# Kernel tuning notes

Measured on AMD Instinct MI355X. Metric: run time of the kernel, lower is better.

## Reference

```python
import jax, jax.numpy as jnp
import numpy as np

HEADS, DIM_HEAD, BITS = 12, 64, 4


def quantize(q, bits):
    # per-tensor affine fake-quant, exactly as the torch quantize()
    s = (q.max() - q.min()) / (2.0 ** bits - 1.0)
    z = jnp.round(2.0 ** bits - 1.0 - q.max() / s)
    return jnp.round(q / s + z), s, z


def setup_inputs() -> dict:
    key = jax.random.key(0)
    k1, k2, k3, k4 = jax.random.split(key, 4)
    return {
        "x": jax.random.normal(k1, (4, 1024, 768), jnp.float32),
        "w_qkv": jax.random.normal(k2, (2304, 768), jnp.float32) * 0.02,  # torch Linear weight [out,in]
        "w_out": jax.random.normal(k3, (768, 768), jnp.float32) * 0.02,
        "b_out": jax.random.normal(k4, (768,), jnp.float32) * 0.02,
    }


def reference(x, w_qkv, w_out, b_out):
    scale = DIM_HEAD ** -0.5
    B, N, D = x.shape
    # --- quantized QKV projection: x @ W^T with zero-point correction ---
    xq, sx1, zx1 = quantize(x, BITS)
    w1, sw1, zw1 = quantize(w_qkv.T, BITS)  # [D, 3*inner]
    xqkv = (xq @ w1
            - w1.sum(0, keepdims=True) * zx1
            - xq.sum(2, keepdims=True) * zw1
            + zx1 * zw1 * D) * (sx1 * sw1)  # [B, N, 3*inner]
    q, k, v = jnp.split(xqkv, 3, axis=-1)
    to_heads = lambda t: t.reshape(B, N, HEADS, DIM_HEAD).transpose(0, 2, 1, 3)  # b h n d
    q, k, v = to_heads(q), to_heads(k), to_heads(v)
    # --- quantized QK^T (note: original omits the +zq*zk*d term) ---
    qq, sq, zq = quantize(q, BITS)
    kq, sk, zk = quantize(k.transpose(0, 1, 3, 2), BITS)  # b h d n
    dots = (qq @ kq
            - kq.sum(2, keepdims=True) * zq
            - qq.sum(3, keepdims=True) * zk) * (scale * sq * sk)  # b h n n
    a = jax.nn.softmax(dots, axis=-1)
    # --- quantized A @ V ---
    aq, sa, za = quantize(a, BITS)
    vq, sv, zv = quantize(v, BITS)
    out = (aq @ vq
           - vq.sum(2, keepdims=True) * za
           - aq.sum(3, keepdims=True) * zv
           + za * zv * N) * (sa * sv)  # b h n d
    out = out.transpose(0, 2, 1, 3).reshape(B, N, HEADS * DIM_HEAD)
    # --- quantized output projection (faithful to original: correction uses
    # xqkv.sum / xqkv width, reproducing the source's use of `x` here) ---
    oq, sx2, zx2 = quantize(out, BITS)
    w2, sw2, zw2 = quantize(w_out.T, BITS)  # [inner, D]
    o = (oq @ w2
         - w2.sum(0, keepdims=True) * zx2
         - xqkv.sum(2, keepdims=True) * zw2
         + zx2 * zw2 * xqkv.shape[2]) * (sx2 * sw2) + b_out
    return o
```

## Files before the change

### kernel.cpp

```cpp
#include <hip/hip_runtime.h>
#include <math.h>

#define HEADS 12
#define DH    64
#define Dm    768
#define I3    2304
#define Nn    1024
#define Mm    4096
#define BHt   48
#define LOG2E 1.4426950408889634f

#define P_X  0
#define P_W1 1
#define P_Q  2
#define P_K  3
#define P_V  4
#define P_A  5
#define P_O  6
#define P_W2 7

typedef int v4i __attribute__((ext_vector_type(4)));

#if __has_builtin(__builtin_amdgcn_exp2f)
#define EXP2(x) __builtin_amdgcn_exp2f(x)
#else
#define EXP2(x) exp2f(x)
#endif

__device__ inline unsigned encf(float f) {
    unsigned u = __float_as_uint(f);
    return (u & 0x80000000u) ? ~u : (u | 0x80000000u);
}
__device__ inline float decf(unsigned u) {
    return (u & 0x80000000u) ? __uint_as_float(u & 0x7fffffffu) : __uint_as_float(~u);
}
__device__ inline void get_sz(const unsigned* scal, int pair, float* s, float* z) {
    float mn = decf(scal[2 * pair]);
    float mx = decf(scal[2 * pair + 1]);
    float ss = (mx - mn) / 15.0f;
    *s = ss;
    *z = rintf(15.0f - mx / ss);
}

__global__ __launch_bounds__(256) void k_init(unsigned* scal, float* z1, int n1, float* z2, int n2) {
    int g = blockIdx.x * 256 + threadIdx.x;
    if (g < n1) z1[g] = 0.f;
    if (g < n2) z2[g] = 0.f;
    if (g < 8) { scal[2 * g] = 0xFFFFFFFFu; scal[2 * g + 1] = 0u; }
}

__global__ __launch_bounds__(256) void k_minmax3(const float* x, const float* w1, const float* w2,
                                                 unsigned* scal) {
    __shared__ float rmn[256], rmx[256];
    int bid = blockIdx.x, tid = threadIdx.x;
    const float* src; int rows, pair, b0, nb;
    if (bid < 256)      { src = x;  rows = 4096; pair = P_X;  b0 = 0;   nb = 256; }
    else if (bid < 384) { src = w1; rows = 2304; pair = P_W1; b0 = 256; nb = 128; }
    else                { src = w2; rows = 768;  pair = P_W2; b0 = 384; nb = 64;  }
    float mn = INFINITY, mx = -INFINITY;
    for (int r = bid - b0; r < rows; r += nb) {
        const float* row = src + (long)r * 768;
#pragma unroll
        for (int k = 0; k < 3; ++k) {
            float v = row[tid + k * 256];
            mn = fminf(mn, v); mx = fmaxf(mx, v);
        }
    }
    rmn[tid] = mn; rmx[tid] = mx; __syncthreads();
    for (int s = 128; s > 0; s >>= 1) {
        if (tid < s) { rmn[tid] = fminf(rmn[tid], rmn[tid + s]); rmx[tid] = fmaxf(rmx[tid], rmx[tid + s]); }
        __syncthreads();
    }
    if (tid == 0) {
        atomicMin(&scal[2 * pair], encf(rmn[0]));
        atomicMax(&scal[2 * pair + 1], encf(rmx[0]));
    }
}

__global__ __launch_bounds__(256) void k_quant3(const float* x, const float* w1, const float* w2,
                                                const unsigned* scal,
                                                signed char* xq, signed char* wq, signed char* w2q,
                                                float* rs_x, float* rs_w1, float* rs_w2) {
    __shared__ float red[256];
    int bid = blockIdx.x, tid = threadIdx.x;
    const float* src; signed char* dq; float* rs; int pair, r;
    if (bid < 4096)      { src = x;  dq = xq;  rs = rs_x;  pair = P_X;  r = bid; }
    else if (bid < 6400) { src = w1; dq = wq;  rs = rs_w1; pair = P_W1; r = bid - 4096; }
    else                 { src = w2; dq = w2q; rs = rs_w2; pair = P_W2; r = bid - 6400; }
    float s, z; get_sz(scal, pair, &s, &z);
    const float* row = src + (long)r * 768;
    signed char* drow = dq + (long)r * 768;
    float acc = 0.f;
#pragma unroll
    for (int k = 0; k < 3; ++k) {
        int c = tid + k * 256;
        float q = rintf(row[c] / s + z);
        drow[c] = (signed char)(int)q;
        acc += q;
    }
    red[tid] = acc; __syncthreads();
    for (int s2 = 128; s2 > 0; s2 >>= 1) { if (tid < s2) red[tid] += red[tid + s2]; __syncthreads(); }
    if (tid == 0) rs[r] = red[0];
}

__global__ __launch_bounds__(256) void k_quant_rows(const float* src, const unsigned* scal, int pair,
                                                    signed char* dq) {
    int r = blockIdx.x, tid = threadIdx.x;
    float s, z; get_sz(scal, pair, &s, &z);
    const float* row = src + (long)r * 768;
    signed char* drow = dq + (long)r * 768;
#pragma unroll
    for (int k = 0; k < 3; ++k) {
        int c = tid + k * 256;
        float q = rintf(row[c] / s + z);
        drow[c] = (signed char)(int)q;
    }
}

__global__ __launch_bounds__(256) void k_gemm_mfma(const signed char* A, const signed char* B,
                                                   const float* colsumB, const float* rowsumA,
                                                   const float* bias, float* C, int K, int ldC,
                                                   const unsigned* scal, int pairA, int pairB,
                                                   float corrK, int do_stats, float* rowsum_out,
                                                   unsigned* scal_mm) {
    __shared__ __align__(16) signed char As[128 * 64];
    __shared__ __align__(16) signed char Bs[128 * 64];
    __shared__ float red[256];
    int tid = threadIdx.x;
    int wave = tid >> 6, lane = tid & 63;
    int col16 = lane & 15, quad = lane >> 4;
    long rowbase = (long)blockIdx.y * 128;
    long colbase = (long)blockIdx.x * 128;

    int c4 = tid & 3, r4 = tid >> 2;
    const signed char* ag0 = A + (rowbase + r4) * K + c4 * 16;
    const signed char* ag1 = A + (rowbase + r4 + 64) * K + c4 * 16;
    const signed char* bg0 = B + (colbase + r4) * K + c4 * 16;
    const signed char* bg1 = B + (colbase + r4 + 64) * K + c4 * 16;
    int soff0 = ((r4 >> 4) << 10) + (c4 << 8) + ((r4 & 15) << 4);
    int soff1 = soff0 + 4096;

    v4i ra0 = *(const v4i*)ag0;
    v4i ra1 = *(const v4i*)ag1;
    v4i rb0 = *(const v4i*)bg0;
    v4i rb1 = *(const v4i*)bg1;

    const int afrag_off = wave * 2048 + quad * 256 + col16 * 16;
    const int bfrag_off = quad * 256 + col16 * 16;
    v4i acc[2][8] = {};
    int nk = K >> 6;
    for (int kt = 0; kt < nk; ++kt) {
        *(v4i*)(As + soff0) = ra0;
        *(v4i*)(As + soff1) = ra1;
        *(v4i*)(Bs + soff0) = rb0;
        *(v4i*)(Bs + soff1) = rb1;
        __syncthreads();
        if (kt + 1 < nk) {
            int ko = (kt + 1) << 6;
            ra0 = *(const v4i*)(ag0 + ko);
            ra1 = *(const v4i*)(ag1 + ko);
            rb0 = *(const v4i*)(bg0 + ko);
            rb1 = *(const v4i*)(bg1 + ko);
        }
        v4i af0 = *(const v4i*)(As + afrag_off);
        v4i af1 = *(const v4i*)(As + afrag_off + 1024);
        v4i bf[8];
#pragma unroll
        for (int g = 0; g < 8; ++g) bf[g] = *(const v4i*)(Bs + bfrag_off + g * 1024);
#pragma unroll
        for (int g = 0; g < 8; ++g) {
            acc[0][g] = __builtin_amdgcn_mfma_i32_16x16x64_i8(af0, bf[g], acc[0][g], 0, 0, 0);
            acc[1][g] = __builtin_amdgcn_mfma_i32_16x16x64_i8(af1, bf[g], acc[1][g], 0, 0, 0);
        }
        __syncthreads();
    }

    float sA, zA, sB, zB;
    get_sz(scal, pairA, &sA, &zA);
    get_sz(scal, pairB, &sB, &zB);
    float sAB = sA * sB;
    float zz = (zA * zB) * corrK;
    float vmn = INFINITY, vmx = -INFINITY;
    float rowpart[2][4] = {};
#pragma unroll
    for (int i2 = 0; i2 < 2; ++i2)
#pragma unroll
        for (int g = 0; g < 8; ++g) {
            long col = colbase + g * 16 + col16;
            float cs = colsumB[col] * zA;
            float bv = bias ? bias[col] : 0.f;
#pragma unroll
            for (int r = 0; r < 4; ++r) {
                long row = rowbase + wave * 32 + i2 * 16 + quad * 4 + r;
                float v = ((float)acc[i2][g][r] - cs - rowsumA[row] * zB + zz) * sAB + bv;
                C[row * ldC + col] = v;
                rowpart[i2][r] += v;
                vmn = fminf(vmn, v); vmx = fmaxf(vmx, v);
            }
        }
    if (do_stats) {
#pragma unroll
        for (int i2 = 0; i2 < 2; ++i2)
#pragma unroll
            for (int r = 0; r < 4; ++r) {
                float s = rowpart[i2][r];
                s += __shfl_xor(s, 1); s += __shfl_xor(s, 2);
                s += __shfl_xor(s, 4); s += __shfl_xor(s, 8);
                if (col16 == 0)
                    atomicAdd(&rowsum_out[rowbase + wave * 32 + i2 * 16 + quad * 4 + r], s);
            }
        int pair = P_Q + (int)(colbase / 768);
        red[tid] = vmx; __syncthreads();
        for (int s = 128; s > 0; s >>= 1) { if (tid < s) red[tid] = fmaxf(red[tid], red[tid + s]); __syncthreads(); }
        if (tid == 0) atomicMax(&scal_mm[2 * pair + 1], encf(red[0]));
        __syncthreads();
        red[tid] = vmn; __syncthreads();
        for (int s = 128; s > 0; s >>= 1) { if (tid < s) red[tid] = fminf(red[tid], red[tid + s]); __syncthreads(); }
        if (tid == 0) atomicMin(&scal_mm[2 * pair], encf(red[0]));
    }
}

__global__ __launch_bounds__(256) void k_quant_qkv2(const float* xqkv, const unsigned* scal,
                                                    signed char* qq, signed char* kq, signed char* vqT,
                                                    float* rowsum_qq, float* cskc, float* colsum_vq) {
    __shared__ __align__(16) signed char vt[64 * 80];
    __shared__ float vred[4][64];
    int blk = blockIdx.x;
    int bh = blk >> 4, itile = blk & 15;
    int tid = threadIdx.x;
    int wave = tid >> 6, d = tid & 63;
    int b = bh / HEADS, h = bh - HEADS * b;
    float sq, zq, sk, zk, sv, zv;
    get_sz(scal, P_Q, &sq, &zq);
    get_sz(scal, P_K, &sk, &zk);
    get_sz(scal, P_V, &sv, &zv);
    float zqcsc2 = zq * ((0.125f * sq) * sk) * LOG2E;
    int vb = 0;
    float vsum = 0.f;
    for (int ir = 0; ir < 16; ++ir) {
        int il = wave * 16 + ir;
        int i = itile * 64 + il;
        const float* row = xqkv + ((long)b * Nn + i) * I3 + h * DH;
        float q = rintf(row[d] / sq + zq);
        float k = rintf(row[768 + d] / sk + zk);
        float v = rintf(row[1536 + d] / sv + zv);
        long o = ((long)bh * Nn + i) * 64 + d;
        qq[o] = (signed char)(int)q;
        kq[o] = (signed char)(int)k;
        vsum += v;
        vb |= ((int)v & 0xff) << ((ir & 3) * 8);
        if ((ir & 3) == 3) {
            *(int*)(vt + d * 80 + (il & ~3)) = vb;
            vb = 0;
        }
        float s1 = q, s2 = k;
        for (int off = 32; off > 0; off >>= 1) {
            s1 += __shfl_down(s1, off);
            s2 += __shfl_down(s2, off);
        }
        if (d == 0) { rowsum_qq[bh * Nn + i] = s1; cskc[bh * Nn + i] = s2 * zqcsc2; }
    }
    vred[wave][d] = vsum;
    __syncthreads();
    int dd = tid >> 2, c = tid & 3;
    *(v4i*)(vqT + ((long)bh * 64 + dd) * 1024 + itile * 64 + c * 16) = *(const v4i*)(vt + dd * 80 + c * 16);
    if (tid < 64)
        atomicAdd(&colsum_vq[bh * 64 + tid],
                  ((vred[0][tid] + vred[1][tid]) + vred[2][tid]) + vred[3][tid]);
}

__global__ __launch_bounds__(256) void k_attn_a8(const signed char* qq, const signed char* kq,
                                                 const float* rowsum_qq, const float* cskc,
                                                 unsigned* scal, float* rowmax, float* sumexp) {
    __shared__ float red[256];
    int blk = blockIdx.x;
    int bh = blk >> 4, itile = blk & 15;
    int tid = threadIdx.x;
    int wave = tid >> 6, lane = tid & 63;
    int col16 = lane & 15, quad = lane >> 4;
    int rowbase = itile * 64 + wave * 16;
    const signed char* kbase = kq + (long)bh * Nn * 64;
    const float* ck = cskc + bh * Nn;
    v4i afrag = *(const v4i*)(qq + ((long)bh * Nn + rowbase + col16) * 64 + quad * 16);
    float sq, zq, sk, zk;
    get_sz(scal, P_Q, &sq, &zq);
    get_sz(scal, P_K, &sk, &zk);
    float csc2 = ((0.125f * sq) * sk) * LOG2E;
    float rzc[4];
#pragma unroll
    for (int r = 0; r < 4; ++r)
        rzc[r] = rowsum_qq[bh * Nn + rowbase + quad * 4 + r] * zk * csc2;
    v4i zero = {0, 0, 0, 0};
    float m[4]    = {-INFINITY, -INFINITY, -INFINITY, -INFINITY};
    float se[4]   = {0.f, 0.f, 0.f, 0.f};
    float lmin[4] = {INFINITY, INFINITY, INFINITY, INFINITY};
    const signed char* kf = kbase + (long)col16 * 64 + quad * 16;
    const float* ckp = ck + col16;
    v4i kb[2][4];
    float ckc[4], ckn[4];
#pragma unroll
    for (int t = 0; t < 4; ++t) {
        kb[0][t] = *(const v4i*)(kf + (long)(t * 16) * 64);
        ckc[t] = ckp[t * 16];
    }
#pragma unroll 2
    for (int ch = 0; ch < 16; ++ch) {
        int cur = ch & 1, nxt = cur ^ 1;
        int pch = (ch < 15) ? ch + 1 : 15;
#pragma unroll
        for (int t = 0; t < 4; ++t) {
            kb[nxt][t] = *(const v4i*)(kf + (long)(pch * 64 + t * 16) * 64);
            ckn[t] = ckp[pch * 64 + t * 16];
        }
#pragma unroll
        for (int t = 0; t < 4; ++t) {
            v4i d = __builtin_amdgcn_mfma_i32_16x16x64_i8(afrag, kb[cur][t], zero, 0, 0, 0);
            float ckv = ckc[t];
#pragma unroll
            for (int r = 0; r < 4; ++r) {
                float dv = fmaf((float)d[r], csc2, -(ckv + rzc[r]));
                lmin[r] = fminf(lmin[r], dv);
                float mn = fmaxf(m[r], dv);
                float e = EXP2(fminf(m[r], dv) - mn);
                se[r] = (dv > m[r]) ? fmaf(se[r], e, 1.0f) : (se[r] + e);
                m[r] = mn;
            }
        }
#pragma unroll
        for (int t = 0; t < 4; ++t) ckc[t] = ckn[t];
    }
#pragma unroll
    for (int r = 0; r < 4; ++r) {
#pragma unroll
        for (int off = 1; off < 16; off <<= 1) {
            float mo = __shfl_xor(m[r], off);
            float so = __shfl_xor(se[r], off);
            float mino = __shfl_xor(lmin[r], off);
            float mn = fmaxf(m[r], mo);
            se[r] = fmaf(se[r], EXP2(m[r] - mn), so * EXP2(mo - mn));
            m[r] = mn;
            lmin[r] = fminf(lmin[r], mino);
        }
    }
    float amax_c = -INFINITY, amin_c = INFINITY;
    if (col16 == 0) {
#pragma unroll
        for (int r = 0; r < 4; ++r) {
            int grow = bh * Nn + rowbase + quad * 4 + r;
            rowmax[grow] = m[r];
            sumexp[grow] = se[r];
            amax_c = fmaxf(amax_c, 1.0f / se[r]);
            amin_c = fminf(amin_c, EXP2(lmin[r] - m[r]) / se[r]);
        }
    }
    red[tid] = amax_c; __syncthreads();
    for (int s = 128; s > 0; s >>= 1) { if (tid < s) red[tid] = fmaxf(red[tid], red[tid + s]); __syncthreads(); }
    if (tid == 0) atomicMax(&scal[2 * P_A + 1], encf(red[0]));
    __syncthreads();
    red[tid] = amin_c; __syncthreads();
    for (int s = 128; s > 0; s >>= 1) { if (tid < s) red[tid] = fminf(red[tid], red[tid + s]); __syncthreads(); }
    if (tid == 0) atomicMin(&scal[2 * P_A], encf(red[0]));
}

__global__ __launch_bounds__(256) void k_attn_b8(const signed char* qq, const signed char* kq,
                                                 const signed char* vqT, const float* rowsum_qq,
                                                 const float* cskc, const float* colsum_vq,
                                                 const float* rowmax, const float* sumexp,
                                                 unsigned* scal, float* out_mat) {
    __shared__ __align__(16) signed char AqB[8192];
    __shared__ float red[256];
    int blk = blockIdx.x;
    int bh = blk >> 4, itile = blk & 15;
    int tid = threadIdx.x;
    int wave = tid >> 6, lane = tid & 63;
    int col16 = lane & 15, quad = lane >> 4;
    int rowbase = itile * 64 + wave * 16;
    int b = bh / HEADS, h = bh - HEADS * b;
    const signed char* kbase = kq + (long)bh * Nn * 64;
    const signed char* vbase = vqT + (long)bh * 64 * 1024;
    const float* ck = cskc + bh * Nn;
    v4i afrag = *(const v4i*)(qq + ((long)bh * Nn + rowbase + col16) * 64 + quad * 16);
    float sq, zq, sk, zk, sv, zv, sa, za;
    get_sz(scal, P_Q, &sq, &zq);
    get_sz(scal, P_K, &sk, &zk);
    get_sz(scal, P_V, &sv, &zv);
    get_sz(scal, P_A, &sa, &za);
    float csc2 = ((0.125f * sq) * sk) * LOG2E;
    float roff[4], crcp[4];
#pragma unroll
    for (int r = 0; r < 4; ++r) {
        int row = bh * Nn + rowbase + quad * 4 + r;
        roff[r] = rowsum_qq[row] * zk * csc2 + rowmax[row];
        crcp[r] = 1.0f / (sumexp[row] * sa);
    }
    v4i accPV[4] = {};
    float rs_a[4] = {0.f, 0.f, 0.f, 0.f};
    v4i zero = {0, 0, 0, 0};
    const signed char* kf = kbase + (long)col16 * 64 + quad * 16;
    const float* ckp = ck + col16;
    const int pa_off = wave * 1024 + col16 * 64 + ((quad ^ (col16 >> 2)) << 4);

    v4i kb0[4], kb1[4];
    float ckr0[4], ckr1[4];
#pragma unroll
    for (int t = 0; t < 4; ++t) {
        kb0[t] = *(const v4i*)(kf + (long)(t * 16) * 64);
        ckr0[t] = ckp[t * 16];
        kb1[t] = *(const v4i*)(kf + (long)(64 + t * 16) * 64);
        ckr1[t] = ckp[64 + t * 16];
    }

#define QUANT_CHUNK(BUF, KB, CKR)                                                       \
    {                                                                                   \
        signed char* myAq = AqB + (BUF) * 4096 + wave * 1024;                           \
        _Pragma("unroll")                                                               \
        for (int t = 0; t < 4; ++t) {                                                   \
            v4i d = __builtin_amdgcn_mfma_i32_16x16x64_i8(afrag, KB[t], zero, 0, 0, 0); \
            float ckv = CKR[t];                                                         \
            int cswz = ((t ^ quad) << 4) + col16;                                       \
            _Pragma("unroll")                                                           \
            for (int r = 0; r < 4; ++r) {                                               \
                float es = fmaf((float)d[r], csc2, -(ckv + roff[r]));                   \
                float fastv = fmaf(EXP2(es), crcp[r], za);                              \
                float aqv = rintf(fastv);                                               \
                rs_a[r] += aqv;                                                         \
                myAq[(quad * 4 + r) * 64 + cswz] = (signed char)(int)aqv;               \
            }                                                                           \
        }                                                                               \
    }

#define BODY(CH, CUR, KBc, CKc, KBn, CKn)                                               \
    {                                                                                   \
        v4i pa = *(const v4i*)(AqB + (CUR) * 4096 + pa_off);                            \
        v4i bv[4];                                                                      \
        _Pragma("unroll")                                                               \
        for (int g = 0; g < 4; ++g)                                                     \
            bv[g] = *(const v4i*)(vbase + (long)(g * 16 + col16) * 1024 + (CH) * 64 + quad * 16); \
        if ((CH) < 14) {                                                                \
            _Pragma("unroll")                                                           \
            for (int t = 0; t < 4; ++t) {                                               \
                KBc[t] = *(const v4i*)(kf + (long)(((CH) + 2) * 64 + t * 16) * 64);     \
                CKc[t] = ckp[((CH) + 2) * 64 + t * 16];                                 \
            }                                                                           \
        }                                                                               \
        if ((CH) < 15) QUANT_CHUNK(1 - (CUR), KBn, CKn)                                 \
        _Pragma("unroll")                                                               \
        for (int g = 0; g < 4; ++g)                                                     \
            accPV[g] = __builtin_amdgcn_mfma_i32_16x16x64_i8(pa, bv[g], accPV[g], 0, 0, 0); \
    }

    QUANT_CHUNK(0, kb0, ckr0)
    for (int ch2 = 0; ch2 < 8; ++ch2) {
        int ch = ch2 * 2;
        BODY(ch, 0, kb0, ckr0, kb1, ckr1)
        BODY(ch + 1, 1, kb1, ckr1, kb0, ckr0)
    }
#undef BODY
#undef QUANT_CHUNK

#pragma unroll
    for (int r = 0; r < 4; ++r)
        for (int off = 1; off < 16; off <<= 1) rs_a[r] += __shfl_xor(rs_a[r], off);
    float sav = sa * sv;
    float zz = (za * zv) * 1024.0f;
    float vmn = INFINITY, vmx = -INFINITY;
#pragma unroll
    for (int g = 0; g < 4; ++g) {
        int d = g * 16 + col16;
        float cs = colsum_vq[bh * 64 + d] * za;
#pragma unroll
        for (int r = 0; r < 4; ++r) {
            int i = rowbase + quad * 4 + r;
            float v = ((float)accPV[g][r] - cs - rs_a[r] * zv + zz) * sav;
            out_mat[((long)b * Nn + i) * Dm + h * DH + d] = v;
            vmn = fminf(vmn, v); vmx = fmaxf(vmx, v);
        }
    }
    red[tid] = vmx; __syncthreads();
    for (int s = 128; s > 0; s >>= 1) { if (tid < s) red[tid] = fmaxf(red[tid], red[tid + s]); __syncthreads(); }
    if (tid == 0) atomicMax(&scal[2 * P_O + 1], encf(red[0]));
    __syncthreads();
    red[tid] = vmn; __syncthreads();
    for (int s = 128; s > 0; s >>= 1) { if (tid < s) red[tid] = fminf(red[tid], red[tid + s]); __syncthreads(); }
    if (tid == 0) atomicMin(&scal[2 * P_O], encf(red[0]));
}

extern "C" void kernel_launch(void* const* d_in, const int* in_sizes, int n_in,
                              void* d_out, int out_size, void* d_ws, size_t ws_size,
                              hipStream_t stream) {
    const float* x     = (const float*)d_in[0];
    const float* w_qkv = (const float*)d_in[1];
    const float* w_out = (const float*)d_in[2];
    const float* b_out = (const float*)d_in[3];

    char* ws = (char*)d_ws;
    size_t off = 0;
    auto alloc = [&](size_t n) -> char* {
        char* p = ws + off;
        off = (off + n + 255) & ~(size_t)255;
        return p;
    };
    unsigned*    scal        = (unsigned*)alloc(64);
    float*       xqkv        = (float*)alloc((size_t)Mm * I3 * 4);
    float*       out_mat     = (float*)alloc((size_t)Mm * Dm * 4);
    signed char* xq          = (signed char*)alloc((size_t)Mm * Dm);
    signed char* wq          = (signed char*)alloc((size_t)I3 * Dm);
    signed char* w2q         = (signed char*)alloc((size_t)Dm * Dm);
    signed char* oq          = (signed char*)alloc((size_t)Mm * Dm);
    signed char* qq          = (signed char*)alloc((size_t)BHt * Nn * DH);
    signed char* kq          = (signed char*)alloc((size_t)BHt * Nn * DH);
    signed char* vqT         = (signed char*)alloc((size_t)BHt * Nn * DH);
    float*       rowsum_xq   = (float*)alloc((size_t)Mm * 4);
    float*       colsum_w1   = (float*)alloc((size_t)I3 * 4);
    float*       colsum_w2   = (float*)alloc((size_t)Dm * 4);
    float*       rowsum_xqkv = (float*)alloc((size_t)Mm * 4);
    float*       rowsum_qq   = (float*)alloc((size_t)BHt * Nn * 4);
    float*       cskc        = (float*)alloc((size_t)BHt * Nn * 4);
    float*       colsum_vq   = (float*)alloc((size_t)BHt * DH * 4);
    float*       rowmax      = (float*)alloc((size_t)BHt * Nn * 4);
    float*       sumexp      = (float*)alloc((size_t)BHt * Nn * 4);

    k_init<<<28, 256, 0, stream>>>(scal, rowsum_xqkv, Mm, colsum_vq, BHt * DH);

    k_minmax3<<<448, 256, 0, stream>>>(x, w_qkv, w_out, scal);
    k_quant3<<<7168, 256, 0, stream>>>(x, w_qkv, w_out, scal, xq, wq, w2q,
                                       rowsum_xq, colsum_w1, colsum_w2);

    {
        dim3 g(I3 / 128, Mm / 128);
        k_gemm_mfma<<<g, 256, 0, stream>>>(xq, wq, colsum_w1, rowsum_xq, nullptr, xqkv,
                                           Dm, I3, scal, P_X, P_W1, 768.0f,
                                           1, rowsum_xqkv, scal);
    }

    k_quant_qkv2<<<BHt * 16, 256, 0, stream>>>(xqkv, scal, qq, kq, vqT,
                                               rowsum_qq, cskc, colsum_vq);

    k_attn_a8<<<BHt * 16, 256, 0, stream>>>(qq, kq, rowsum_qq, cskc, scal, rowmax, sumexp);
    k_attn_b8<<<BHt * 16, 256, 0, stream>>>(qq, kq, vqT, rowsum_qq, cskc, colsum_vq,
                                            rowmax, sumexp, scal, out_mat);

    k_quant_rows<<<Mm, 256, 0, stream>>>(out_mat, scal, P_O, oq);

    {
        dim3 g(Dm / 128, Mm / 128);
        k_gemm_mfma<<<g, 256, 0, stream>>>(oq, w2q, colsum_w2, rowsum_xqkv, b_out, (float*)d_out,
                                           Dm, Dm, scal, P_O, P_W2, 2304.0f,
                                           0, nullptr, nullptr);
    }
}
```

Baseline: 255.6 us.

## Split attention key range across wave pairs and double attention grid size

Both attention kernels now give each block 32 query rows instead of 64, with two waves per 16-row strip each covering half of the key columns. Partial softmax statistics and partial PV accumulators are merged through shared memory, which doubles the grid to 1536 blocks and halves the serial key loop per wave. Launch bounds now request higher occupancy. The cost is duplicated Q fragment loads, extra LDS traffic and barriers for the merge, and half the waves sitting idle during the output store.

```diff
diff --git a/kernel.cpp b/kernel.cpp
--- a/kernel.cpp
+++ b/kernel.cpp
@@ -269,16 +269,18 @@
                   ((vred[0][tid] + vred[1][tid]) + vred[2][tid]) + vred[3][tid]);
 }
 
-__global__ __launch_bounds__(256) void k_attn_a8(const signed char* qq, const signed char* kq,
+__global__ __launch_bounds__(256, 6) void k_attn_a8(const signed char* qq, const signed char* kq,
                                                  const float* rowsum_qq, const float* cskc,
                                                  unsigned* scal, float* rowmax, float* sumexp) {
     __shared__ float red[256];
+    __shared__ float Am[4][16], Ase[4][16], Almn[4][16];
     int blk = blockIdx.x;
-    int bh = blk >> 4, itile = blk & 15;
+    int bh = blk >> 5, itile = blk & 31;
     int tid = threadIdx.x;
     int wave = tid >> 6, lane = tid & 63;
     int col16 = lane & 15, quad = lane >> 4;
-    int rowbase = itile * 64 + wave * 16;
+    int rowbase = itile * 32 + (wave >> 1) * 16;
+    int c0 = (wave & 1) * 8;
     const signed char* kbase = kq + (long)bh * Nn * 64;
     const float* ck = cskc + bh * Nn;
     v4i afrag = *(const v4i*)(qq + ((long)bh * Nn + rowbase + col16) * 64 + quad * 16);
@@ -294,8 +296,8 @@
     float m[4]    = {-INFINITY, -INFINITY, -INFINITY, -INFINITY};
     float se[4]   = {0.f, 0.f, 0.f, 0.f};
     float lmin[4] = {INFINITY, INFINITY, INFINITY, INFINITY};
-    const signed char* kf = kbase + (long)col16 * 64 + quad * 16;
-    const float* ckp = ck + col16;
+    const signed char* kf = kbase + (long)(c0 * 64 + col16) * 64 + quad * 16;
+    const float* ckp = ck + c0 * 64 + col16;
     v4i kb[2][4];
     float ckc[4], ckn[4];
 #pragma unroll
@@ -304,9 +306,9 @@
         ckc[t] = ckp[t * 16];
     }
 #pragma unroll 2
-    for (int ch = 0; ch < 16; ++ch) {
+    for (int ch = 0; ch < 8; ++ch) {
         int cur = ch & 1, nxt = cur ^ 1;
-        int pch = (ch < 15) ? ch + 1 : 15;
+        int pch = (ch < 7) ? ch + 1 : 7;
 #pragma unroll
         for (int t = 0; t < 4; ++t) {
             kb[nxt][t] = *(const v4i*)(kf + (long)(pch * 64 + t * 16) * 64);
@@ -342,16 +344,27 @@
             lmin[r] = fminf(lmin[r], mino);
         }
     }
+    if (col16 == 0) {
+#pragma unroll
+        for (int r = 0; r < 4; ++r) {
+            Am[wave][quad * 4 + r]   = m[r];
+            Ase[wave][quad * 4 + r]  = se[r];
+            Almn[wave][quad * 4 + r] = lmin[r];
+        }
+    }
+    __syncthreads();
     float amax_c = -INFINITY, amin_c = INFINITY;
-    if (col16 == 0) {
-#pragma unroll
-        for (int r = 0; r < 4; ++r) {
-            int grow = bh * Nn + rowbase + quad * 4 + r;
-            rowmax[grow] = m[r];
-            sumexp[grow] = se[r];
-            amax_c = fmaxf(amax_c, 1.0f / se[r]);
-            amin_c = fminf(amin_c, EXP2(lmin[r] - m[r]) / se[r]);
-        }
+    if (tid < 32) {
+        int p = tid >> 4, row = tid & 15;
+        float m1 = Am[2 * p][row], m2 = Am[2 * p + 1][row];
+        float mm = fmaxf(m1, m2);
+        float ses = Ase[2 * p][row] * EXP2(m1 - mm) + Ase[2 * p + 1][row] * EXP2(m2 - mm);
+        float lmn = fminf(Almn[2 * p][row], Almn[2 * p + 1][row]);
+        int grow = bh * Nn + itile * 32 + p * 16 + row;
+        rowmax[grow] = mm;
+        sumexp[grow] = ses;
+        amax_c = 1.0f / ses;
+        amin_c = EXP2(lmn - mm) / ses;
     }
     red[tid] = amax_c; __syncthreads();
     for (int s = 128; s > 0; s >>= 1) { if (tid < s) red[tid] = fmaxf(red[tid], red[tid + s]); __syncthreads(); }
@@ -362,19 +375,23 @@
     if (tid == 0) atomicMin(&scal[2 * P_A], encf(red[0]));
 }
 
-__global__ __launch_bounds__(256) void k_attn_b8(const signed char* qq, const signed char* kq,
+__global__ __launch_bounds__(256, 6) void k_attn_b8(const signed char* qq, const signed char* kq,
                                                  const signed char* vqT, const float* rowsum_qq,
                                                  const float* cskc, const float* colsum_vq,
                                                  const float* rowmax, const float* sumexp,
                                                  unsigned* scal, float* out_mat) {
     __shared__ __align__(16) signed char AqB[8192];
     __shared__ float red[256];
+    __shared__ int   mrgI[2][16][64];
+    __shared__ float mrgF[2][4][64];
     int blk = blockIdx.x;
-    int bh = blk >> 4, itile = blk & 15;
+    int bh = blk >> 5, itile = blk & 31;
     int tid = threadIdx.x;
     int wave = tid >> 6, lane = tid & 63;
     int col16 = lane & 15, quad = lane >> 4;
-    int rowbase = itile * 64 + wave * 16;
+    int rowbase = itile * 32 + (wave >> 1) * 16;
+    int jhalf = wave & 1;
+    int c0 = jhalf * 8;
     int b = bh / HEADS, h = bh - HEADS * b;
     const signed char* kbase = kq + (long)bh * Nn * 64;
     const signed char* vbase = vqT + (long)bh * 64 * 1024;
@@ -396,8 +413,8 @@
     v4i accPV[4] = {};
     float rs_a[4] = {0.f, 0.f, 0.f, 0.f};
     v4i zero = {0, 0, 0, 0};
-    const signed char* kf = kbase + (long)col16 * 64 + quad * 16;
-    const float* ckp = ck + col16;
+    const signed char* kf = kbase + (long)(c0 * 64 + col16) * 64 + quad * 16;
+    const float* ckp = ck + c0 * 64 + col16;
     const int pa_off = wave * 1024 + col16 * 64 + ((quad ^ (col16 >> 2)) << 4);
 
     v4i kb0[4], kb1[4];
@@ -435,28 +452,49 @@
         v4i bv[4];                                                                      \
         _Pragma("unroll")                                                               \
         for (int g = 0; g < 4; ++g)                                                     \
-            bv[g] = *(const v4i*)(vbase + (long)(g * 16 + col16) * 1024 + (CH) * 64 + quad * 16); \
-        if ((CH) < 14) {                                                                \
+            bv[g] = *(const v4i*)(vbase + (long)(g * 16 + col16) * 1024 + (c0 + (CH)) * 64 + quad * 16); \
+        if ((CH) < 6) {                                                                 \
             _Pragma("unroll")                                                           \
             for (int t = 0; t < 4; ++t) {                                               \
                 KBc[t] = *(const v4i*)(kf + (long)(((CH) + 2) * 64 + t * 16) * 64);     \
                 CKc[t] = ckp[((CH) + 2) * 64 + t * 16];                                 \
             }                                                                           \
         }                                                                               \
-        if ((CH) < 15) QUANT_CHUNK(1 - (CUR), KBn, CKn)                                 \
+        if ((CH) < 7) QUANT_CHUNK(1 - (CUR), KBn, CKn)                                  \
         _Pragma("unroll")                                                               \
         for (int g = 0; g < 4; ++g)                                                     \
             accPV[g] = __builtin_amdgcn_mfma_i32_16x16x64_i8(pa, bv[g], accPV[g], 0, 0, 0); \
     }
 
     QUANT_CHUNK(0, kb0, ckr0)
-    for (int ch2 = 0; ch2 < 8; ++ch2) {
+    for (int ch2 = 0; ch2 < 4; ++ch2) {
         int ch = ch2 * 2;
         BODY(ch, 0, kb0, ckr0, kb1, ckr1)
         BODY(ch + 1, 1, kb1, ckr1, kb0, ckr0)
     }
 #undef BODY
 #undef QUANT_CHUNK
+
+    __syncthreads();
+    if (jhalf) {
+        int p = wave >> 1;
+#pragma unroll
+        for (int g = 0; g < 4; ++g)
+#pragma unroll
+            for (int r = 0; r < 4; ++r) mrgI[p][g * 4 + r][lane] = accPV[g][r];
+#pragma unroll
+        for (int r = 0; r < 4; ++r) mrgF[p][r][lane] = rs_a[r];
+    }
+    __syncthreads();
+    if (!jhalf) {
+        int p = wave >> 1;
+#pragma unroll
+        for (int g = 0; g < 4; ++g)
+#pragma unroll
+            for (int r = 0; r < 4; ++r) accPV[g][r] += mrgI[p][g * 4 + r][lane];
+#pragma unroll
+        for (int r = 0; r < 4; ++r) rs_a[r] += mrgF[p][r][lane];
+    }
 
 #pragma unroll
     for (int r = 0; r < 4; ++r)
@@ -464,16 +502,18 @@
     float sav = sa * sv;
     float zz = (za * zv) * 1024.0f;
     float vmn = INFINITY, vmx = -INFINITY;
-#pragma unroll
-    for (int g = 0; g < 4; ++g) {
-        int d = g * 16 + col16;
-        float cs = colsum_vq[bh * 64 + d] * za;
-#pragma unroll
-        for (int r = 0; r < 4; ++r) {
-            int i = rowbase + quad * 4 + r;
-            float v = ((float)accPV[g][r] - cs - rs_a[r] * zv + zz) * sav;
-            out_mat[((long)b * Nn + i) * Dm + h * DH + d] = v;
-            vmn = fminf(vmn, v); vmx = fmaxf(vmx, v);
+    if (!jhalf) {
+#pragma unroll
+        for (int g = 0; g < 4; ++g) {
+            int d = g * 16 + col16;
+            float cs = colsum_vq[bh * 64 + d] * za;
+#pragma unroll
+            for (int r = 0; r < 4; ++r) {
+                int i = rowbase + quad * 4 + r;
+                float v = ((float)accPV[g][r] - cs - rs_a[r] * zv + zz) * sav;
+                out_mat[((long)b * Nn + i) * Dm + h * DH + d] = v;
+                vmn = fminf(vmn, v); vmx = fmaxf(vmx, v);
+            }
         }
     }
     red[tid] = vmx; __syncthreads();
@@ -536,8 +576,8 @@
     k_quant_qkv2<<<BHt * 16, 256, 0, stream>>>(xqkv, scal, qq, kq, vqT,
                                                rowsum_qq, cskc, colsum_vq);
 
-    k_attn_a8<<<BHt * 16, 256, 0, stream>>>(qq, kq, rowsum_qq, cskc, scal, rowmax, sumexp);
-    k_attn_b8<<<BHt * 16, 256, 0, stream>>>(qq, kq, vqT, rowsum_qq, cskc, colsum_vq,
+    k_attn_a8<<<BHt * 32, 256, 0, stream>>>(qq, kq, rowsum_qq, cskc, scal, rowmax, sumexp);
+    k_attn_b8<<<BHt * 32, 256, 0, stream>>>(qq, kq, vqT, rowsum_qq, cskc, colsum_vq,
                                             rowmax, sumexp, scal, out_mat);
 
     k_quant_rows<<<Mm, 256, 0, stream>>>(out_mat, scal, P_O, oq);
```

Measured after the change: 305.9 us. 19.7% more time.
